# Kernel optimization log

Measured on AMD Instinct MI355X. Metric: run time of the kernel, lower is better.

Reference implementation:

```python
import jax, jax.numpy as jnp
import numpy as np

N_QUBITS = 10
N_LAYERS = 4
BATCH = 8192
DIM = 2 ** N_QUBITS


def setup_inputs() -> dict:
    key = jax.random.key(0)
    k1, k2 = jax.random.split(key)
    x = jax.random.normal(k1, (BATCH, N_QUBITS), dtype=jnp.float32)
    weights = jax.random.normal(k2, (N_LAYERS, N_QUBITS, 3), dtype=jnp.float32) * 0.1
    return {"x": x, "weights": weights}


def _apply_1q(state, U, q):
    """Apply shared 2x2 gate U to qubit q (wire 0 = most significant bit)."""
    B = state.shape[0]
    s = state.reshape(B, 2 ** q, 2, -1)
    s = jnp.einsum('ij,bajc->baic', U, s)
    return s.reshape(B, -1)


def _apply_1q_batched(state, U, q):
    """Apply per-sample 2x2 gates U[b] to qubit q."""
    B = state.shape[0]
    s = state.reshape(B, 2 ** q, 2, -1)
    s = jnp.einsum('bij,bajc->baic', U, s)
    return s.reshape(B, -1)


def _apply_cnot(state, c, t):
    """CNOT with control c, target t."""
    B = state.shape[0]
    s = state.reshape((B,) + (2,) * N_QUBITS)
    c_ax, t_ax = c + 1, t + 1
    ctrl0 = jnp.take(s, 0, axis=c_ax)
    ctrl1 = jnp.take(s, 1, axis=c_ax)
    # after removing control axis, target axis shifts down if it was after control
    t_ax2 = t_ax - 1 if t_ax > c_ax else t_ax
    ctrl1 = jnp.flip(ctrl1, axis=t_ax2)  # X on target when control=1
    s = jnp.stack([ctrl0, ctrl1], axis=c_ax)
    return s.reshape(B, -1)


def _rot_matrix(phi, theta, omega):
    """PennyLane Rot(phi,theta,omega) = RZ(omega) RY(theta) RZ(phi)."""
    c = jnp.cos(theta / 2)
    s = jnp.sin(theta / 2)
    e = lambda a: jnp.exp(1j * a)
    row0 = jnp.stack([e(-(phi + omega) / 2) * c, -e((phi - omega) / 2) * s])
    row1 = jnp.stack([e(-(phi - omega) / 2) * s, e((phi + omega) / 2) * c])
    return jnp.stack([row0, row1]).astype(jnp.complex64)


def _circuit(x, weights):
    B = x.shape[0]
    state = jnp.zeros((B, DIM), jnp.complex64).at[:, 0].set(1.0)
    # angle encoding: RY(x[:, q]) on each wire, batched over samples
    for q in range(N_QUBITS):
        a = x[:, q] / 2
        c, s = jnp.cos(a), jnp.sin(a)
        U = jnp.stack([jnp.stack([c, -s], -1), jnp.stack([s, c], -1)], -2)
        state = _apply_1q_batched(state, U.astype(jnp.complex64), q)
    for l in range(N_LAYERS):
        for q in range(N_QUBITS):
            U = _rot_matrix(weights[l, q, 0], weights[l, q, 1], weights[l, q, 2])
            state = _apply_1q(state, U, q)
        for q in range(N_QUBITS - 1):
            state = _apply_cnot(state, q, q + 1)
        if N_QUBITS > 2:
            state = _apply_cnot(state, N_QUBITS - 1, 0)
    # <Z_q> = sum_{bit_q=0} |amp|^2 - sum_{bit_q=1} |amp|^2
    probs = jnp.real(state) ** 2 + jnp.imag(state) ** 2
    outs = []
    for q in range(N_QUBITS):
        p = probs.reshape(B, 2 ** q, 2, -1)
        outs.append(p[:, :, 0, :].sum((1, 2)) - p[:, :, 1, :].sum((1, 2)))
    return jnp.stack(outs, axis=-1)  # [B, n_qubits]


def reference(x, weights):
    return _circuit(x, weights)
```

## Files before the change

### kernel.cpp

```cpp
#include <hip/hip_runtime.h>
#include <math.h>

#define NQ 10
#define NL 4

typedef float v2f __attribute__((ext_vector_type(2)));

template<int CTRL>
__device__ __forceinline__ float dppx(float v) {
  return __int_as_float(__builtin_amdgcn_update_dpp(0, __float_as_int(v), CTRL, 0xF, 0xF, true));
}
template<int OFF>
__device__ __forceinline__ float swzx(float v) {
  return __int_as_float(__builtin_amdgcn_ds_swizzle(__float_as_int(v), OFF));
}
__device__ __forceinline__ void pl16swap(float &a, float &b) {
  asm("v_permlane16_swap_b32 %0, %1" : "+v"(a), "+v"(b));
}
__device__ __forceinline__ void pl32swap(float &a, float &b) {
  asm("v_permlane32_swap_b32 %0, %1" : "+v"(a), "+v"(b));
}

template<int LB>
__device__ __forceinline__ float part(float v) {
  if constexpr (LB == 0) return dppx<0xB1>(v);
  else if constexpr (LB == 1) return dppx<0x4E>(v);
  else if constexpr (LB == 2) return swzx<0x101F>(v);
  else return swzx<0x201F>(v);
}

__device__ __forceinline__ v2f cmul(v2f u, v2f a) {
  v2f d;
  asm("v_pk_mul_f32 %0, %1, %2 op_sel_hi:[0,1]\n\t"
      "v_pk_fma_f32 %0, %1, %2, %0 op_sel:[1,1,0] op_sel_hi:[1,0,1] neg_lo:[0,1,0]"
      : "=&v"(d) : "v"(u), "v"(a));
  return d;
}
__device__ __forceinline__ void cfma(v2f &d, v2f u, v2f a) {
  asm("v_pk_fma_f32 %0, %1, %2, %0 op_sel_hi:[0,1,1]\n\t"
      "v_pk_fma_f32 %0, %1, %2, %0 op_sel:[1,1,0] op_sel_hi:[1,0,1] neg_lo:[0,1,0]"
      : "+v"(d) : "v"(u), "v"(a));
}

template<int RB>
__device__ __forceinline__ void gate_rbit(v2f a[16], v2f u00, v2f u01, v2f u10, v2f u11) {
#pragma unroll
  for (int r0 = 0; r0 < 16; ++r0) {
    if ((r0 >> RB) & 1) continue;
    const int r1 = r0 | (1 << RB);
    const v2f a0 = a[r0], a1 = a[r1];
    v2f n0 = cmul(u00, a0); cfma(n0, u01, a1);
    v2f n1 = cmul(u10, a0); cfma(n1, u11, a1);
    a[r0] = n0;
    a[r1] = n1;
  }
}

template<int LB>
__device__ __forceinline__ void gate_part(v2f a[16], v2f cS, v2f cP) {
#pragma unroll
  for (int h = 0; h < 4; ++h) {
    v2f p[4];
#pragma unroll
    for (int k = 0; k < 4; ++k) {
      const int r = h * 4 + k;
      p[k].x = part<LB>(a[r].x);
      p[k].y = part<LB>(a[r].y);
    }
#pragma unroll
    for (int k = 0; k < 4; ++k) {
      const int r = h * 4 + k;
      v2f n = cmul(cS, a[r]); cfma(n, cP, p[k]);
      a[r] = n;
    }
  }
}

template<bool IS32>
__device__ __forceinline__ void gate_swap(v2f a[16], v2f cL, v2f cH) {
#pragma unroll
  for (int r = 0; r < 16; ++r) {
    float lx = a[r].x, hx = a[r].x;
    float ly = a[r].y, hy = a[r].y;
    if constexpr (IS32) { pl32swap(lx, hx); pl32swap(ly, hy); }
    else                { pl16swap(lx, hx); pl16swap(ly, hy); }
    v2f lo, hi;
    lo.x = lx; lo.y = ly;
    hi.x = hx; hi.y = hy;
    v2f n = cmul(cL, lo); cfma(n, cH, hi);
    a[r] = n;
  }
}

__device__ __forceinline__ void ring_comp(v2f a[16], int addr0, int addr1, bool odd) {
  float B[16];
#pragma unroll
  for (int g = 0; g < 16; ++g) {
    const int par = ((g ^ (g >> 1) ^ (g >> 2) ^ (g >> 3)) & 1);
    B[g] = __int_as_float(__builtin_amdgcn_ds_bpermute(par ? addr1 : addr0,
                                                       __float_as_int(a[g].x)));
  }
#pragma unroll
  for (int r = 0; r < 16; ++r) {
    const int g = (r ^ (r >> 1));
    a[r].x = odd ? B[g ^ 12] : B[g];
  }
#pragma unroll
  for (int g = 0; g < 16; ++g) {
    const int par = ((g ^ (g >> 1) ^ (g >> 2) ^ (g >> 3)) & 1);
    B[g] = __int_as_float(__builtin_amdgcn_ds_bpermute(par ? addr1 : addr0,
                                                       __float_as_int(a[g].y)));
  }
#pragma unroll
  for (int r = 0; r < 16; ++r) {
    const int g = (r ^ (r >> 1));
    a[r].y = odd ? B[g ^ 12] : B[g];
  }
}

__device__ __forceinline__ float wsum(float v) {
  v += dppx<0xB1>(v);
  v += dppx<0x4E>(v);
  v += swzx<0x101F>(v);
  v += swzx<0x201F>(v);
  { float a = v, b = v; pl16swap(a, b); v = a + b; }
  { float a = v, b = v; pl32swap(a, b); v = a + b; }
  return v;
}

__device__ __forceinline__ void encode(const float* __restrict__ xb, int lane, v2f a[16]) {
  float lfac;
  {
    float c, s, h;
    h = 0.5f * xb[9]; s = __sinf(h); c = __cosf(h); lfac  = ((lane >> 0) & 1) ? s : c;
    h = 0.5f * xb[8]; s = __sinf(h); c = __cosf(h); lfac *= ((lane >> 1) & 1) ? s : c;
    h = 0.5f * xb[7]; s = __sinf(h); c = __cosf(h); lfac *= ((lane >> 2) & 1) ? s : c;
    h = 0.5f * xb[6]; s = __sinf(h); c = __cosf(h); lfac *= ((lane >> 3) & 1) ? s : c;
    h = 0.5f * xb[5]; s = __sinf(h); c = __cosf(h); lfac *= ((lane >> 4) & 1) ? s : c;
    h = 0.5f * xb[4]; s = __sinf(h); c = __cosf(h); lfac *= ((lane >> 5) & 1) ? s : c;
  }
  const float h0 = 0.5f * xb[0], h1 = 0.5f * xb[1], h2 = 0.5f * xb[2], h3 = 0.5f * xb[3];
  const float s0 = __sinf(h0), c0 = __cosf(h0);
  const float s1 = __sinf(h1), c1 = __cosf(h1);
  const float s2 = __sinf(h2), c2 = __cosf(h2);
  const float s3 = __sinf(h3), c3 = __cosf(h3);
#pragma unroll
  for (int r = 0; r < 16; ++r) {
    float f = lfac;
    f *= ((r >> 0) & 1) ? s3 : c3;
    f *= ((r >> 1) & 1) ? s2 : c2;
    f *= ((r >> 2) & 1) ? s1 : c1;
    f *= ((r >> 3) & 1) ? s0 : c0;
    a[r].x = f;
    a[r].y = 0.f;
  }
}

__global__ __launch_bounds__(256) void qsim_kernel(const float* __restrict__ x,
                                                   const float* __restrict__ w,
                                                   float* __restrict__ out,
                                                   int batch) {
  __shared__ __align__(16) float gsh[NL * NQ * 8];
  const int tid = threadIdx.x;
  if (tid < NL * NQ) {
    const float phi = w[tid * 3 + 0];
    const float th  = w[tid * 3 + 1];
    const float om  = w[tid * 3 + 2];
    const float c  = __cosf(0.5f * th),          s  = __sinf(0.5f * th);
    const float cp = __cosf(-0.5f * (phi + om)), sp = __sinf(-0.5f * (phi + om));
    const float cm = __cosf(0.5f * (phi - om)),  sm = __sinf(0.5f * (phi - om));
    float* g = &gsh[tid * 8];
    g[0] = cp * c;  g[1] = sp * c;
    g[2] = -cm * s; g[3] = -sm * s;
    g[4] = cm * s;  g[5] = -sm * s;
    g[6] = cp * c;  g[7] = -sp * c;
  }
  __syncthreads();

  const int samp = (int)(blockIdx.x * (blockDim.x >> 6)) + (tid >> 6);
  const int lane = tid & 63;
  if (samp >= batch) return;

  const int addr0 = 4 * (lane ^ (lane >> 1));
  const int addr1 = addr0 ^ 128;
  const bool lodd = (lane & 1);

  v2f a[16];
  encode(x + samp * NQ, lane, a);

#pragma unroll
  for (int l = 0; l < NL; ++l) {
    const float* gl = &gsh[l * NQ * 8];

#pragma unroll
    for (int q = 0; q < 4; ++q) {
      const v2f* gv = (const v2f*)(gl + q * 8);
      const v2f u00 = gv[0], u01 = gv[1], u10 = gv[2], u11 = gv[3];
      if (q == 0)      gate_rbit<3>(a, u00, u01, u10, u11);
      else if (q == 1) gate_rbit<2>(a, u00, u01, u10, u11);
      else if (q == 2) gate_rbit<1>(a, u00, u01, u10, u11);
      else             gate_rbit<0>(a, u00, u01, u10, u11);
    }
    {
      const v2f* gv = (const v2f*)(gl + 4 * 8);
      const bool hb = (lane >> 5) & 1;
      gate_swap<true>(a, hb ? gv[2] : gv[0], hb ? gv[3] : gv[1]);
    }
    {
      const v2f* gv = (const v2f*)(gl + 5 * 8);
      const bool hb = (lane >> 4) & 1;
      gate_swap<false>(a, hb ? gv[2] : gv[0], hb ? gv[3] : gv[1]);
    }
#pragma unroll
    for (int q = 6; q < 10; ++q) {
      const v2f* gv = (const v2f*)(gl + q * 8);
      const bool hb = (lane >> (9 - q)) & 1;
      const v2f cS = hb ? gv[3] : gv[0];
      const v2f cP = hb ? gv[2] : gv[1];
      if (q == 6)      gate_part<3>(a, cS, cP);
      else if (q == 7) gate_part<2>(a, cS, cP);
      else if (q == 8) gate_part<1>(a, cS, cP);
      else             gate_part<0>(a, cS, cP);
    }

    ring_comp(a, addr0, addr1, lodd);
  }

  float p[16];
#pragma unroll
  for (int r = 0; r < 16; ++r) p[r] = a[r].x * a[r].x + a[r].y * a[r].y;

  float z03[4];
#pragma unroll
  for (int q = 0; q < 4; ++q) {
    const int rb = 3 - q;
    float acc = 0.f;
#pragma unroll
    for (int r = 0; r < 16; ++r) acc += ((r >> rb) & 1) ? -p[r] : p[r];
    z03[q] = wsum(acc);
  }

  float P = 0.f;
#pragma unroll
  for (int r = 0; r < 16; ++r) P += p[r];
  const float sg0 = (lane & 1)  ? -1.f : 1.f;
  const float sg1 = (lane & 2)  ? -1.f : 1.f;
  const float sg2 = (lane & 4)  ? -1.f : 1.f;
  const float sg3 = (lane & 8)  ? -1.f : 1.f;
  const float sg4 = (lane & 16) ? -1.f : 1.f;
  const float sg5 = (lane & 32) ? -1.f : 1.f;
  float v = P;
  v = __builtin_fmaf(sg0, v, dppx<0xB1>(v));
  v = __builtin_fmaf(sg1, v, dppx<0x4E>(v));
  v = __builtin_fmaf(sg2, v, swzx<0x101F>(v));
  v = __builtin_fmaf(sg3, v, swzx<0x201F>(v));
  { float xx = v, yy = v; pl16swap(xx, yy); v = __builtin_fmaf(sg4, yy, xx); }
  { float xx = v, yy = v; pl32swap(xx, yy); v = __builtin_fmaf(sg5, yy, xx); }

  if (lane == 0) {
    out[samp * NQ + 0] = z03[0];
    out[samp * NQ + 1] = z03[1];
    out[samp * NQ + 2] = z03[2];
    out[samp * NQ + 3] = z03[3];
  } else if ((lane & (lane - 1)) == 0) {
    const int lb = __ffs(lane) - 1;
    out[samp * NQ + (9 - lb)] = v;
  }
}

extern "C" void kernel_launch(void* const* d_in, const int* in_sizes, int n_in,
                              void* d_out, int out_size, void* d_ws, size_t ws_size,
                              hipStream_t stream) {
  const float* x = (const float*)d_in[0];
  const float* w = (const float*)d_in[1];
  float* out = (float*)d_out;
  const int batch = in_sizes[0] / NQ;
  const int waves_per_block = 256 / 64;
  const int grid = (batch + waves_per_block - 1) / waves_per_block;
  hipLaunchKernelGGL(qsim_kernel, dim3(grid), dim3(256), 0, stream, x, w, out, batch);
}
```

Before: 132.2 us.

## Skip final CNOT ring by folding its parity map into Z measurements

```diff
diff --git a/kernel.cpp b/kernel.cpp
--- a/kernel.cpp
+++ b/kernel.cpp
@@ -223,33 +223,34 @@
       else             gate_part<0>(a, cS, cP);
     }
 
-    ring_comp(a, addr0, addr1, lodd);
+    if (l < NL - 1) ring_comp(a, addr0, addr1, lodd);
   }
 
   float p[16];
 #pragma unroll
   for (int r = 0; r < 16; ++r) p[r] = a[r].x * a[r].x + a[r].y * a[r].y;
 
-  float z03[4];
-#pragma unroll
-  for (int q = 0; q < 4; ++q) {
-    const int rb = 3 - q;
-    float acc = 0.f;
-#pragma unroll
-    for (int r = 0; r < 16; ++r) acc += ((r >> rb) & 1) ? -p[r] : p[r];
-    z03[q] = wsum(acc);
-  }
-
-  float P = 0.f;
-#pragma unroll
-  for (int r = 0; r < 16; ++r) P += p[r];
+  float S7 = 0.f, S12 = 0.f, S14 = 0.f, S15 = 0.f;
+#pragma unroll
+  for (int r = 0; r < 16; ++r) {
+    const float pr = p[r];
+    S7  += (__builtin_popcount(r & 7)  & 1) ? -pr : pr;
+    S12 += (__builtin_popcount(r & 12) & 1) ? -pr : pr;
+    S14 += (__builtin_popcount(r & 14) & 1) ? -pr : pr;
+    S15 += (__builtin_popcount(r & 15) & 1) ? -pr : pr;
+  }
+
+  const float z0 = wsum((__popc(lane) & 1) ? -S7 : S7);
+  const float z1 = wsum(S12);
+  const float z2 = wsum(S14);
+
   const float sg0 = (lane & 1)  ? -1.f : 1.f;
   const float sg1 = (lane & 2)  ? -1.f : 1.f;
   const float sg2 = (lane & 4)  ? -1.f : 1.f;
   const float sg3 = (lane & 8)  ? -1.f : 1.f;
   const float sg4 = (lane & 16) ? -1.f : 1.f;
   const float sg5 = (lane & 32) ? -1.f : 1.f;
-  float v = P;
+  float v = S15;
   v = __builtin_fmaf(sg0, v, dppx<0xB1>(v));
   v = __builtin_fmaf(sg1, v, dppx<0x4E>(v));
   v = __builtin_fmaf(sg2, v, swzx<0x101F>(v));
@@ -258,14 +259,16 @@
   { float xx = v, yy = v; pl32swap(xx, yy); v = __builtin_fmaf(sg5, yy, xx); }
 
   if (lane == 0) {
-    out[samp * NQ + 0] = z03[0];
-    out[samp * NQ + 1] = z03[1];
-    out[samp * NQ + 2] = z03[2];
-    out[samp * NQ + 3] = z03[3];
-  } else if ((lane & (lane - 1)) == 0) {
-    const int lb = __ffs(lane) - 1;
-    out[samp * NQ + (9 - lb)] = v;
-  }
+    out[samp * NQ + 0] = z0;
+    out[samp * NQ + 1] = z1;
+    out[samp * NQ + 2] = z2;
+    out[samp * NQ + 3] = v;
+  } else if (lane == 32) out[samp * NQ + 4] = v;
+  else if (lane == 48)   out[samp * NQ + 5] = v;
+  else if (lane == 56)   out[samp * NQ + 6] = v;
+  else if (lane == 60)   out[samp * NQ + 7] = v;
+  else if (lane == 62)   out[samp * NQ + 8] = v;
+  else if (lane == 63)   out[samp * NQ + 9] = v;
 }
 
 extern "C" void kernel_launch(void* const* d_in, const int* in_sizes, int n_in,
```

Measured after the change: 114.6 us (median of 3 runs). 1.15x faster.
